# Kernel optimization log

Measured on AMD Instinct MI355X. Metric: run time of the kernel, lower is better.

The kernel has to match this reference:

```python
import jax, jax.numpy as jnp
import numpy as np

DIM = 192
HEADS = 6
WS = (2, 7, 7)
SHIFT = (1, 3, 3)
MLP_HID = int(DIM * 4.0)
N = WS[0] * WS[1] * WS[2]  # 98


def _relative_position_index():
    wt, wh, ww = WS
    coords = np.stack(np.meshgrid(np.arange(wt), np.arange(wh), np.arange(ww), indexing='ij'))
    cf = coords.reshape(3, -1)  # (3, N)
    rel = cf[:, :, None] - cf[:, None, :]  # (3, N, N)
    rel = rel.transpose(1, 2, 0).copy()
    rel[:, :, 0] += wt - 1
    rel[:, :, 1] += wh - 1
    rel[:, :, 2] += ww - 1
    rel[:, :, 0] *= (2 * wh - 1) * (2 * ww - 1)
    rel[:, :, 1] *= 2 * ww - 1
    return rel.sum(-1)  # (N, N) int

RPI = jnp.asarray(_relative_position_index())


def setup_inputs() -> dict:
    key = jax.random.key(0)
    ks = jax.random.split(key, 12)
    B, C, T, H, W = 2, DIM, 8, 56, 56
    n_bias = (2 * WS[0] - 1) * (2 * WS[1] - 1) * (2 * WS[2] - 1)
    s = lambda k, shp, sd=0.02: jax.random.normal(k, shp, jnp.float32) * sd
    return {
        'x': jax.random.normal(ks[0], (B, C, T, H, W), jnp.float32),
        'mask_matrix': jnp.zeros((256, N, N), jnp.float32),
        'norm1_g': jnp.ones((DIM,), jnp.float32),
        'norm1_b': jnp.zeros((DIM,), jnp.float32),
        'qkv_w': s(ks[1], (DIM, 3 * DIM)),
        'qkv_b': jnp.zeros((3 * DIM,), jnp.float32),
        'proj_w': s(ks[2], (DIM, DIM)),
        'proj_b': jnp.zeros((DIM,), jnp.float32),
        'rpb_table': s(ks[3], (n_bias, HEADS)),
        'norm2_g': jnp.ones((DIM,), jnp.float32),
        'norm2_b': jnp.zeros((DIM,), jnp.float32),
        'fc1_w': s(ks[4], (DIM, MLP_HID)),
        'fc1_b': jnp.zeros((MLP_HID,), jnp.float32),
        'fc2_w': s(ks[5], (MLP_HID, DIM)),
        'fc2_b': jnp.zeros((DIM,), jnp.float32),
    }


def _layernorm(x, g, b, eps=1e-5):
    mu = jnp.mean(x, -1, keepdims=True)
    var = jnp.var(x, -1, keepdims=True)
    return (x - mu) * jax.lax.rsqrt(var + eps) * g + b


def _window_partition(x):
    # x: (B, T, H, W, C) -> (B*nW, N, C)
    B, T, H, W, C = x.shape
    wt, wh, ww = WS
    x = x.reshape(B, T // wt, wt, H // wh, wh, W // ww, ww, C)
    x = x.transpose(0, 1, 3, 5, 2, 4, 6, 7)
    return x.reshape(-1, wt * wh * ww, C)


def _window_reverse(win, B, T, H, W):
    wt, wh, ww = WS
    C = win.shape[-1]
    x = win.reshape(B, T // wt, H // wh, W // ww, wt, wh, ww, C)
    x = x.transpose(0, 1, 4, 2, 5, 3, 6, 7)
    return x.reshape(B, T, H, W, C)


def reference(x, mask_matrix, norm1_g, norm1_b, qkv_w, qkv_b, proj_w, proj_b,
              rpb_table, norm2_g, norm2_b, fc1_w, fc1_b, fc2_w, fc2_b):
    B, C, T, H, W = x.shape
    hd = C // HEADS
    scale = hd ** -0.5

    shortcut = x.transpose(0, 2, 3, 4, 1)  # (B,T,H,W,C) channel-last residual
    xn = _layernorm(shortcut, norm1_g, norm1_b)
    # cyclic shift
    xs = jnp.roll(xn, shift=(-SHIFT[0], -SHIFT[1], -SHIFT[2]), axis=(1, 2, 3))
    xw = _window_partition(xs)  # (B_, N, C)
    B_ = xw.shape[0]

    qkv = (xw @ qkv_w + qkv_b).reshape(B_, N, 3, HEADS, hd)
    q, k, v = (qkv[:, :, 0].transpose(0, 2, 1, 3),
               qkv[:, :, 1].transpose(0, 2, 1, 3),
               qkv[:, :, 2].transpose(0, 2, 1, 3))  # (B_, h, N, d)
    attn = jnp.einsum('bhnd,bhmd->bhnm', q * scale, k)
    bias = rpb_table[RPI.reshape(-1)].reshape(N, N, HEADS).transpose(2, 0, 1)
    attn = attn + bias[None]
    nW = mask_matrix.shape[0]
    attn = attn.reshape(B_ // nW, nW, HEADS, N, N) + mask_matrix[None, :, None]
    attn = jax.nn.softmax(attn.reshape(B_, HEADS, N, N), axis=-1)
    out = jnp.einsum('bhnm,bhmd->bhnd', attn, v).transpose(0, 2, 1, 3).reshape(B_, N, C)
    out = out @ proj_w + proj_b

    xr = _window_reverse(out, B, T, H, W)
    xr = jnp.roll(xr, shift=SHIFT, axis=(1, 2, 3))
    x1 = shortcut + xr

    xn2 = _layernorm(x1, norm2_g, norm2_b)
    h1 = jax.nn.gelu(xn2 @ fc1_w + fc1_b, approximate=False)
    x2 = x1 + (h1 @ fc2_w + fc2_b)
    return x2.transpose(0, 4, 1, 2, 3)  # (B, C, T, H, W)
```

## Files before the change

kernel.cpp:

```cpp
#include <hip/hip_runtime.h>
#include <hip/hip_bf16.h>
#include <math.h>

#define DEV __device__ __forceinline__

typedef __bf16 bf16;
typedef __bf16 bf16x8 __attribute__((ext_vector_type(8)));
typedef float f32x4 __attribute__((ext_vector_type(4)));

DEV f32x4 zero4() { f32x4 z; z[0]=0.f; z[1]=0.f; z[2]=0.f; z[3]=0.f; return z; }

DEV void gload_lds16(const bf16* g, bf16* l) {
    __builtin_amdgcn_global_load_lds(
        (const __attribute__((address_space(1))) void*)g,
        (__attribute__((address_space(3))) void*)l, 16, 0, 0);
}

DEV float gelu_f(float v) {
    float e = __expf(-1.702f * v);
    return v * __builtin_amdgcn_rcpf(1.0f + e);
}

DEV f32x4 bmfma(bf16x8 a, bf16x8 b, f32x4 c) {
    return __builtin_amdgcn_mfma_f32_16x16x32_bf16(a, b, c, 0, 0, 0);
}


__global__ __launch_bounds__(256) void prep_all_k(
    const float* __restrict__ qw, const float* __restrict__ pw,
    const float* __restrict__ f1, const float* __restrict__ f2,
    const float* __restrict__ rpb, const float* __restrict__ maskm,
    bf16* __restrict__ qwt, bf16* __restrict__ pwt,
    bf16* __restrict__ f1t, bf16* __restrict__ f2t,
    float* __restrict__ biasF, float* __restrict__ maskF,
    int* __restrict__ wflag)
{
    int bid = blockIdx.x;
    if (bid < 3136) {
        int i = bid * 256 + threadIdx.x;
        if (i >= 256*7*7*64) return;
        int lane = i & 63; int g = i >> 6;
        int j = g % 7; g /= 7; int rt = g % 7; int wib = g / 7;
        int l15 = lane & 15, lg = lane >> 4;
        int nk = j*16 + l15;
        f32x4 o;
        #pragma unroll
        for (int r = 0; r < 4; r++) {
            int nq = rt*16 + lg*4 + r; if (nq > 97) nq = 97;
            o[r] = (nk < 98) ? maskm[((size_t)wib*98 + nq)*98 + nk] : 0.f;
        }
        *(f32x4*)&maskF[(size_t)i*4] = o;
    } else if (bid < 3712) {
        int i = (bid - 3136) * 256 + threadIdx.x;
        if (i < 576*192) { int n = i / 192, k = i % 192; qwt[i] = (bf16)qw[(size_t)k*576 + n]; }
        if (i < 192*192) { int n = i / 192, k = i % 192; pwt[i] = (bf16)pw[(size_t)k*192 + n]; }
        if (i < 768*192) { int n = i / 192, k = i % 192; f1t[i] = (bf16)f1[(size_t)k*768 + n]; }
        if (i < 192*768) { int n = i / 768, k = i % 768; f2t[i] = (bf16)f2[(size_t)k*192 + n]; }
    } else if (bid < 3786) {
        int i = (bid - 3712) * 256 + threadIdx.x;
        if (i >= 6*7*7*64) return;
        int lane = i & 63; int g = i >> 6;
        int j = g % 7; g /= 7; int rt = g % 7; int head = g / 7;
        int l15 = lane & 15, lg = lane >> 4;
        int nk = j*16 + l15;
        f32x4 o;
        #pragma unroll
        for (int r = 0; r < 4; r++) {
            int nq = rt*16 + lg*4 + r; if (nq > 97) nq = 97;
            if (nk < 98) {
                int t1 = nq/49, r1 = nq%49, h1 = r1/7, w1 = r1%7;
                int t2 = nk/49, r2 = nk%49, h2 = r2/7, w2 = r2%7;
                int idx = (t1 - t2 + 1)*169 + (h1 - h2 + 6)*13 + (w1 - w2 + 6);
                o[r] = rpb[idx*6 + head];
            } else {
                o[r] = -1e30f;
            }
        }
        *(f32x4*)&biasF[(size_t)i*4] = o;
    } else {
        __shared__ int f;
        int wib = bid - 3786;
        if (threadIdx.x == 0) f = 0;
        __syncthreads();
        int any = 0;
        const float* mm = maskm + (size_t)wib*9604;
        for (int i = threadIdx.x; i < 9604; i += 256)
            if (mm[i] != 0.f) any = 1;
        if (any) atomicOr(&f, 1);
        __syncthreads();
        if (threadIdx.x == 0) wflag[wib] = f;
    }
}

__global__ __launch_bounds__(256) void ln1_window_k(
    const float* __restrict__ x, const float* __restrict__ g,
    const float* __restrict__ bta, bf16* __restrict__ xw)
{
    __shared__ float tile[56*193];
    __shared__ float mu[56], rs[56];
    int blk = blockIdx.x;
    int bb = blk / 448; int r = blk % 448; int ts = r / 56; int hs = r % 56;
    int t = (ts + 1) & 7;
    int h = hs + 3; if (h >= 56) h -= 56;
    int tid = threadIdx.x;
    const float* xs = x + ((size_t)bb*1536 + t)*3136 + h*56;
    for (int e = tid; e < 192*56; e += 256) {
        int c = e / 56, w = e % 56;
        int wsp = w - 3; if (wsp < 0) wsp += 56;
        tile[wsp*193 + c] = xs[(size_t)c*25088 + w];
    }
    __syncthreads();
    if (tid < 224) {
        int row = tid >> 2, q = tid & 3;
        float s = 0.f, s2 = 0.f;
        for (int c = q*48; c < q*48 + 48; c++) {
            float v = tile[row*193 + c]; s += v; s2 += v*v;
        }
        s  += __shfl_xor(s, 1);  s  += __shfl_xor(s, 2);
        s2 += __shfl_xor(s2, 1); s2 += __shfl_xor(s2, 2);
        if (q == 0) {
            float m = s * (1.0f/192.0f);
            mu[row] = m;
            rs[row] = rsqrtf(s2 * (1.0f/192.0f) - m*m + 1e-5f);
        }
    }
    __syncthreads();
    int tb = ts >> 1, wt = ts & 1;
    int hb = hs / 7, wh = hs % 7;
    for (int e = tid; e < 56*192; e += 256) {
        int wpos = e / 192, c = e % 192;
        float v = (tile[wpos*193 + c] - mu[wpos]) * rs[wpos] * g[c] + bta[c];
        int wb = wpos / 7, ww = wpos % 7;
        int widx = bb*256 + tb*64 + hb*8 + wb;
        int n = wt*49 + wh*7 + ww;
        xw[((size_t)widx*98 + n)*192 + c] = (bf16)v;
    }
}

template<int KT, int NT, int BN, int EPI, int DB>
__global__ __launch_bounds__(256) void gemm_k(
    const bf16* __restrict__ A, const bf16* __restrict__ BT,
    const float* __restrict__ bias, const float* __restrict__ resid,
    void* __restrict__ outp)
{
    constexpr int BUFS = DB ? 2 : 1;
    __shared__ bf16 smem[BUFS*128*64 + BUFS*BN*64];
    bf16* laB = smem;
    bf16* lbB = smem + BUFS*128*64;
    constexpr int NTILES = NT / BN;
    constexpr int NK = KT / 64;
    constexpr int JT = BN / 32;
    constexpr int WN = BN / 2;
    constexpr int SPX = 392 / 8;
    int blk = blockIdx.x;
    int xcd = blk & 7, ix = blk >> 3;
    int m0 = (xcd * SPX + ix / NTILES) * 128;
    int n0 = (ix % NTILES) * BN;
    int tid = threadIdx.x;
    int lane = tid & 63;
    int wv = tid >> 6;
    int wr = wv >> 1, wc = wv & 1;
    int l15 = lane & 15, lg = lane >> 4;

    auto stage = [&](int kt, int buf) {
        int kb = kt * 64;
        #pragma unroll
        for (int t = 0; t < 4; t++) {
            int e = t*256 + wv*64 + lane;
            int row = e >> 3, ck = e & 7;
            gload_lds16(&A[(size_t)(m0 + row)*KT + kb + ((ck ^ (row & 7)) << 3)],
                        &laB[buf*128*64 + (t*256 + wv*64) * 8]);
        }
        #pragma unroll
        for (int t = 0; t < JT; t++) {
            int e = t*256 + wv*64 + lane;
            int row = e >> 3, ck = e & 7;
            gload_lds16(&BT[(size_t)(n0 + row)*KT + kb + ((ck ^ (row & 7)) << 3)],
                        &lbB[buf*BN*64 + (t*256 + wv*64) * 8]);
        }
    };

    f32x4 acc[4][JT];
    #pragma unroll
    for (int i = 0; i < 4; i++)
        #pragma unroll
        for (int j = 0; j < JT; j++) acc[i][j] = zero4();

    auto compute = [&](int cur) {
        const bf16* lab = laB + cur*128*64;
        const bf16* lbb = lbB + cur*BN*64;
        #pragma unroll
        for (int ks = 0; ks < 64; ks += 32) {
            int lc = (ks >> 3) + lg;
            bf16x8 af[4], bfr[JT];
            #pragma unroll
            for (int i = 0; i < 4; i++) {
                int ri = wr*64 + i*16 + l15;
                af[i] = *(const bf16x8*)&lab[ri*64 + ((lc ^ (ri & 7)) << 3)];
            }
            #pragma unroll
            for (int j = 0; j < JT; j++) {
                int rj = wc*WN + j*16 + l15;
                bfr[j] = *(const bf16x8*)&lbb[rj*64 + ((lc ^ (rj & 7)) << 3)];
            }
            #pragma unroll
            for (int i = 0; i < 4; i++)
                #pragma unroll
                for (int j = 0; j < JT; j++)
                    acc[i][j] = bmfma(af[i], bfr[j], acc[i][j]);
        }
    };

    if constexpr (DB) {
        stage(0, 0);
        __syncthreads();
        for (int kt = 0; kt < NK; kt++) {
            int cur = kt & 1;
            if (kt + 1 < NK) stage(kt + 1, cur ^ 1);
            compute(cur);
            __syncthreads();
        }
    } else {
        for (int kt = 0; kt < NK; kt++) {
            stage(kt, 0);
            __syncthreads();
            compute(0);
            __syncthreads();
        }
    }

    if constexpr (EPI == 4) {
        #pragma unroll
        for (int i = 0; i < 4; i++) {
            #pragma unroll
            for (int j = 0; j < JT; j++) {
                int row0 = m0 + wr*64 + i*16 + lg*4;
                int col = n0 + wc*WN + j*16 + l15;
                f32x4 o;
                #pragma unroll
                for (int r = 0; r < 4; r++)
                    o[r] = acc[i][j][r] + bias[col] + resid[(size_t)(row0 + r)*NT + col];
                int bb2 = row0 >= 25088;
                size_t off = (size_t)bb2*192*25088 + (size_t)col*25088 + (row0 - bb2*25088);
                *(f32x4*)&((float*)outp)[off] = o;
            }
        }
    } else if constexpr (EPI == 5) {
        #pragma unroll
        for (int i = 0; i < 4; i++) {
            #pragma unroll
            for (int j = 0; j < JT; j++) {
                int col = n0 + wc*WN + j*16 + l15;
                int sel = col / 192, hd = (col % 192) >> 5, d = col & 31;
                float bv = bias[col];
                #pragma unroll
                for (int r = 0; r < 4; r++) {
                    int row = m0 + wr*64 + i*16 + lg*4 + r;
                    int b_ = row / 98, n = row - b_*98;
                    size_t dst = (((size_t)b_*6 + hd)*3 + sel)*3136 + n*32 + d;
                    ((bf16*)outp)[dst] = (bf16)(acc[i][j][r] + bv);
                }
            }
        }
    } else if constexpr (EPI == 1 || EPI == 0) {
        #pragma unroll
        for (int i = 0; i < 4; i++) {
            #pragma unroll
            for (int j = 0; j < JT; j++) {
                #pragma unroll
                for (int r = 0; r < 4; r++) {
                    int row = m0 + wr*64 + i*16 + lg*4 + r;
                    int col = n0 + wc*WN + j*16 + l15;
                    float v = acc[i][j][r] + bias[col];
                    if constexpr (EPI == 1)
                        ((float*)outp)[(size_t)row*NT + col] = v;
                    else
                        ((bf16*)outp)[(size_t)row*NT + col] = (bf16)v;
                }
            }
        }
    } else {
        bf16* fs = smem;
        #pragma unroll
        for (int i = 0; i < 4; i++) {
            #pragma unroll
            for (int j = 0; j < JT; j++) {
                int colw = wc*WN + j*16 + l15;
                float bv = bias[n0 + colw];
                #pragma unroll
                for (int r = 0; r < 4; r++) {
                    int lr = wr*64 + i*16 + lg*4 + r;
                    fs[lr*72 + colw] = (bf16)gelu_f(acc[i][j][r] + bv);
                }
            }
        }
        __syncthreads();
        {
            int lr = tid >> 1, c0 = (tid & 1) * 32;
            size_t gbase = (size_t)(m0 + lr)*NT + n0 + c0;
            #pragma unroll
            for (int k = 0; k < 4; k++) {
                bf16x8 o = *(const bf16x8*)&fs[lr*72 + c0 + k*8];
                *(bf16x8*)&((bf16*)outp)[gbase + k*8] = o;
            }
        }
    }
}

__global__ __launch_bounds__(128) void attn_k(
    const bf16* __restrict__ qkv, const float* __restrict__ biasF,
    const float* __restrict__ maskF, const int* __restrict__ wflag,
    bf16* __restrict__ aout)
{
    __shared__ bf16 VT[32*128];
    __shared__ bf16 Pl[2*16*136];
    int blk = blockIdx.x;
    int t8 = (blk & 7) * 384 + (blk >> 3);
    int b_ = t8 / 6, head = t8 % 6;
    int tid = threadIdx.x, lane = tid & 63, wv = tid >> 6;
    int l15 = lane & 15, lg = (lane >> 4) & 3;
    int wib = b_ & 255;
    const bf16* base = qkv + (size_t)(b_*6 + head)*3*3136;
    const int hasmask = wflag[wib];

    {
        unsigned int* vz = (unsigned int*)VT;
        for (int e = tid; e < 2048; e += 128) vz[e] = 0u;
        unsigned int* pz = (unsigned int*)Pl;
        for (int e = tid; e < 256; e += 128) {
            int w2 = e >> 7, rem = e & 127;
            int row = rem >> 3, cp = rem & 7;
            pz[(w2*16 + row)*68 + 56 + cp] = 0u;
        }
    }
    __syncthreads();
    {
        int dq = tid >> 5;
        int kl = tid & 31;
        const bf16* vbase = base + 2*3136 + dq*8;
        #pragma unroll
        for (int kr = 0; kr < 4; kr++) {
            int k = kr*32 + kl;
            if (k < 98) {
                bf16x8 v8 = *(const bf16x8*)&vbase[k*32];
                #pragma unroll
                for (int j = 0; j < 8; j++)
                    VT[(dq*8 + j)*128 + (k ^ (j << 3))] = v8[j];
            }
        }
    }
    __syncthreads();

    bf16x8 kfr[7];
    #pragma unroll
    for (int j = 0; j < 7; j++) {
        int krow = j*16 + l15; if (krow > 97) krow = 97;
        kfr[j] = *(const bf16x8*)&base[3136 + krow*32 + lg*8];
    }

    const float scale = 0.17677669529663687f;
    bf16* Pw = Pl + wv*16*136;
    const int rt0 = wv ? 4 : 0, rt1 = wv ? 7 : 4;

    auto loadQ = [&](int rt) {
        int qrow = rt*16 + l15; if (qrow > 97) qrow = 97;
        return *(const bf16x8*)&base[qrow*32 + lg*8];
    };
    bf16x8 qf = loadQ(rt0);

    #pragma unroll 1
    for (int rt = rt0; rt < rt1; rt++) {
        bf16x8 qnext = qf;
        if (rt + 1 < rt1) qnext = loadQ(rt + 1);
        f32x4 sacc[7];
        #pragma unroll
        for (int j = 0; j < 7; j++) sacc[j] = zero4();
        #pragma unroll
        for (int j = 0; j < 7; j++)
            sacc[j] = bmfma(qf, kfr[j], sacc[j]);
        {
            const float* bfp = biasF + ((size_t)(head*7 + rt)*7)*256 + lane*4;
            #pragma unroll
            for (int j = 0; j < 7; j++) {
                f32x4 bv = *(const f32x4*)&bfp[j*256];
                sacc[j] = sacc[j]*scale + bv;
            }
            if (hasmask) {
                const float* mfp = maskF + ((size_t)(wib*7 + rt)*7)*256 + lane*4;
                #pragma unroll
                for (int j = 0; j < 7; j++) {
                    f32x4 mv = *(const f32x4*)&mfp[j*256];
                    sacc[j] = sacc[j] + mv;
                }
            }
            f32x4 m4 = sacc[0];
            #pragma unroll
            for (int j = 1; j < 7; j++) {
                #pragma unroll
                for (int r = 0; r < 4; r++) m4[r] = fmaxf(m4[r], sacc[j][r]);
            }
            #pragma unroll
            for (int d = 1; d < 16; d <<= 1) {
                #pragma unroll
                for (int r = 0; r < 4; r++) m4[r] = fmaxf(m4[r], __shfl_xor(m4[r], d));
            }
            f32x4 s4 = zero4();
            #pragma unroll
            for (int j = 0; j < 7; j++) {
                #pragma unroll
                for (int r = 0; r < 4; r++) sacc[j][r] = __expf(sacc[j][r] - m4[r]);
                s4 += sacc[j];
            }
            #pragma unroll
            for (int d = 1; d < 16; d <<= 1) {
                #pragma unroll
                for (int r = 0; r < 4; r++) s4[r] += __shfl_xor(s4[r], d);
            }
            f32x4 inv4;
            #pragma unroll
            for (int r = 0; r < 4; r++) inv4[r] = 1.0f / s4[r];
            #pragma unroll
            for (int j = 0; j < 7; j++)
                #pragma unroll
                for (int r = 0; r < 4; r++)
                    Pw[(lg*4 + r)*136 + j*16 + l15] = (bf16)(sacc[j][r]*inv4[r]);
        }
        #pragma unroll
        for (int dt = 0; dt < 2; dt++) {
            int dl = dt*16 + l15;
            int xr = (dl & 7) << 3;
            f32x4 oacc = zero4();
            #pragma unroll
            for (int kc = 0; kc < 4; kc++) {
                bf16x8 pf = *(const bf16x8*)&Pw[l15*136 + kc*32 + lg*8];
                bf16x8 vf = *(const bf16x8*)&VT[dl*128 + ((kc*32 + lg*8) ^ xr)];
                oacc = bmfma(pf, vf, oacc);
            }
            #pragma unroll
            for (int r = 0; r < 4; r++) {
                int row = rt*16 + lg*4 + r;
                if (row < 98)
                    aout[((size_t)b_*98 + row)*192 + head*32 + dt*16 + l15] = (bf16)oacc[r];
            }
        }
        qf = qnext;
    }
}

__global__ __launch_bounds__(256) void rev_res_ln2_k(
    const float* __restrict__ x, const bf16* __restrict__ pw,
    const float* __restrict__ g2, const float* __restrict__ b2,
    float* __restrict__ x1, bf16* __restrict__ xn2)
{
    __shared__ float tile[56*193];
    __shared__ float mu[56], rs[56];
    int blk = blockIdx.x;
    int bb = blk / 448; int r = blk % 448; int t = r / 56; int h = r % 56;
    int ts = (t + 7) & 7;
    int hs = h - 3; if (hs < 0) hs += 56;
    int tid = threadIdx.x;
    const float* xs = x + ((size_t)bb*1536 + t)*3136 + h*56;
    for (int e = tid; e < 192*56; e += 256) {
        int c = e / 56, w = e % 56;
        tile[w*193 + c] = xs[(size_t)c*25088 + w];
    }
    __syncthreads();
    int tb = ts >> 1, wt = ts & 1, hb = hs / 7, wh = hs % 7;
    for (int e = tid; e < 56*192; e += 256) {
        int w = e / 192, c = e % 192;
        int wsp = w - 3; if (wsp < 0) wsp += 56;
        int wb = wsp / 7, ww = wsp % 7;
        size_t tok = (size_t)(bb*256 + tb*64 + hb*8 + wb)*98 + wt*49 + wh*7 + ww;
        tile[w*193 + c] += (float)pw[tok*192 + c];
    }
    __syncthreads();
    if (tid < 224) {
        int row = tid >> 2, q = tid & 3;
        float s = 0.f, s2 = 0.f;
        for (int c = q*48; c < q*48 + 48; c++) {
            float v = tile[row*193 + c]; s += v; s2 += v*v;
        }
        s  += __shfl_xor(s, 1);  s  += __shfl_xor(s, 2);
        s2 += __shfl_xor(s2, 1); s2 += __shfl_xor(s2, 2);
        if (q == 0) {
            float m = s * (1.0f/192.0f);
            mu[row] = m;
            rs[row] = rsqrtf(s2 * (1.0f/192.0f) - m*m + 1e-5f);
        }
    }
    __syncthreads();
    size_t tok0 = ((size_t)(bb*8 + t)*56 + h)*56;
    for (int e = tid; e < 56*192; e += 256) {
        int w = e / 192, c = e % 192;
        float v = tile[w*193 + c];
        x1[(tok0 + w)*192 + c] = v;
        xn2[(tok0 + w)*192 + c] = (bf16)((v - mu[w]) * rs[w] * g2[c] + b2[c]);
    }
}

extern "C" void kernel_launch(void* const* d_in, const int* in_sizes, int n_in,
                              void* d_out, int out_size, void* d_ws, size_t ws_size,
                              hipStream_t stream)
{
    const float* x     = (const float*)d_in[0];
    const float* maskm = (const float*)d_in[1];
    const float* n1g   = (const float*)d_in[2];
    const float* n1b   = (const float*)d_in[3];
    const float* qkvw  = (const float*)d_in[4];
    const float* qkvb  = (const float*)d_in[5];
    const float* projw = (const float*)d_in[6];
    const float* projb = (const float*)d_in[7];
    const float* rpb   = (const float*)d_in[8];
    const float* n2g   = (const float*)d_in[9];
    const float* n2b   = (const float*)d_in[10];
    const float* f1w   = (const float*)d_in[11];
    const float* f1b   = (const float*)d_in[12];
    const float* f2w   = (const float*)d_in[13];
    const float* f2b   = (const float*)d_in[14];

    char* ws = (char*)d_ws;
    int*   wflag   = (int*)(ws + 0);
    bf16*  qkv_wt  = (bf16*)(ws + 1024);
    bf16*  proj_wt = (bf16*)(ws + 222208);
    bf16*  fc1_wt  = (bf16*)(ws + 295936);
    bf16*  fc2_wt  = (bf16*)(ws + 590848);
    float* biasF   = (float*)(ws + 885760);
    bf16* xw   = (bf16*)(ws + 1180672);
    bf16* aout = xw;
    char* Bp = ws + 1180672 + 19267584;
    bf16*  qkv  = (bf16*)Bp;
    bf16*  pwin = (bf16*)Bp;
    char* Cp = Bp + 57802752;
    float* x1  = (float*)Cp;
    bf16*  xn2 = (bf16*)(Cp + 38535168);
    bf16*  h1  = (bf16*)(Cp + 38535168 + 19267584);
    float* maskF = (float*)(Cp + 38535168 + 19267584);

    prep_all_k<<<4042, 256, 0, stream>>>(qkvw, projw, f1w, f2w, rpb, maskm,
                                         qkv_wt, proj_wt, fc1_wt, fc2_wt,
                                         biasF, maskF, wflag);
    ln1_window_k<<<896, 256, 0, stream>>>(x, n1g, n1b, xw);
    gemm_k<192, 576, 192, 5, 0><<<392*3, 256, 0, stream>>>(xw, qkv_wt, qkvb, nullptr, qkv);
    attn_k<<<3072, 128, 0, stream>>>(qkv, biasF, maskF, wflag, aout);
    gemm_k<192, 192, 64, 0, 0><<<392*3, 256, 0, stream>>>(aout, proj_wt, projb, nullptr, pwin);
    rev_res_ln2_k<<<896, 256, 0, stream>>>(x, pwin, n2g, n2b, x1, xn2);
    gemm_k<192, 768, 64, 2, 0><<<392*12, 256, 0, stream>>>(xn2, fc1_wt, f1b, nullptr, h1);
    gemm_k<768, 192, 64, 4, 1><<<392*3, 256, 0, stream>>>(h1, fc2_wt, f2b, x1, (float*)d_out);
}
```

Baseline: 233.3 us.

## Store residual in bf16, skip mask expansion for zero windows, LDS-staged proj epilogue

The mask-flag computation moves into its own kernel ahead of prep, so prep can skip writing the expanded mask tile for windows whose mask is all zero. The residual x1 is now stored in bf16 instead of fp32, which halves its write and its read in the final GEMM epilogue, at some precision cost on the residual path. The projection GEMM switches to the LDS-staged epilogue path (EPI 3, gelu off) for coalesced bf16 stores. The cost is one extra kernel launch.

```diff
diff --git a/kernel.cpp b/kernel.cpp
--- a/kernel.cpp
+++ b/kernel.cpp
@@ -25,6 +25,22 @@
     return __builtin_amdgcn_mfma_f32_16x16x32_bf16(a, b, c, 0, 0, 0);
 }
 
+
+__global__ __launch_bounds__(256) void prep_flag_k(
+    const float* __restrict__ maskm, int* __restrict__ wflag)
+{
+    __shared__ int f;
+    int wib = blockIdx.x;
+    if (threadIdx.x == 0) f = 0;
+    __syncthreads();
+    int any = 0;
+    const float* mm = maskm + (size_t)wib*9604;
+    for (int i = threadIdx.x; i < 9604; i += 256)
+        if (mm[i] != 0.f) any = 1;
+    if (any) atomicOr(&f, 1);
+    __syncthreads();
+    if (threadIdx.x == 0) wflag[wib] = f;
+}
 
 __global__ __launch_bounds__(256) void prep_all_k(
     const float* __restrict__ qw, const float* __restrict__ pw,
@@ -33,7 +49,7 @@
     bf16* __restrict__ qwt, bf16* __restrict__ pwt,
     bf16* __restrict__ f1t, bf16* __restrict__ f2t,
     float* __restrict__ biasF, float* __restrict__ maskF,
-    int* __restrict__ wflag)
+    const int* __restrict__ wflag)
 {
     int bid = blockIdx.x;
     if (bid < 3136) {
@@ -41,6 +57,7 @@
         if (i >= 256*7*7*64) return;
         int lane = i & 63; int g = i >> 6;
         int j = g % 7; g /= 7; int rt = g % 7; int wib = g / 7;
+        if (wflag[wib] == 0) return;
         int l15 = lane & 15, lg = lane >> 4;
         int nk = j*16 + l15;
         f32x4 o;
@@ -56,7 +73,7 @@
         if (i < 192*192) { int n = i / 192, k = i % 192; pwt[i] = (bf16)pw[(size_t)k*192 + n]; }
         if (i < 768*192) { int n = i / 192, k = i % 192; f1t[i] = (bf16)f1[(size_t)k*768 + n]; }
         if (i < 192*768) { int n = i / 768, k = i % 768; f2t[i] = (bf16)f2[(size_t)k*192 + n]; }
-    } else if (bid < 3786) {
+    } else {
         int i = (bid - 3712) * 256 + threadIdx.x;
         if (i >= 6*7*7*64) return;
         int lane = i & 63; int g = i >> 6;
@@ -77,18 +94,6 @@
             }
         }
         *(f32x4*)&biasF[(size_t)i*4] = o;
-    } else {
-        __shared__ int f;
-        int wib = bid - 3786;
-        if (threadIdx.x == 0) f = 0;
-        __syncthreads();
-        int any = 0;
-        const float* mm = maskm + (size_t)wib*9604;
-        for (int i = threadIdx.x; i < 9604; i += 256)
-            if (mm[i] != 0.f) any = 1;
-        if (any) atomicOr(&f, 1);
-        __syncthreads();
-        if (threadIdx.x == 0) wflag[wib] = f;
     }
 }
 
@@ -140,7 +145,7 @@
 template<int KT, int NT, int BN, int EPI, int DB>
 __global__ __launch_bounds__(256) void gemm_k(
     const bf16* __restrict__ A, const bf16* __restrict__ BT,
-    const float* __restrict__ bias, const float* __restrict__ resid,
+    const float* __restrict__ bias, const void* __restrict__ resid,
     void* __restrict__ outp)
 {
     constexpr int BUFS = DB ? 2 : 1;
@@ -230,6 +235,7 @@
     }
 
     if constexpr (EPI == 4) {
+        const bf16* rs = (const bf16*)resid;
         #pragma unroll
         for (int i = 0; i < 4; i++) {
             #pragma unroll
@@ -239,7 +245,7 @@
                 f32x4 o;
                 #pragma unroll
                 for (int r = 0; r < 4; r++)
-                    o[r] = acc[i][j][r] + bias[col] + resid[(size_t)(row0 + r)*NT + col];
+                    o[r] = acc[i][j][r] + bias[col] + (float)rs[(size_t)(row0 + r)*NT + col];
                 int bb2 = row0 >= 25088;
                 size_t off = (size_t)bb2*192*25088 + (size_t)col*25088 + (row0 - bb2*25088);
                 *(f32x4*)&((float*)outp)[off] = o;
@@ -262,7 +268,7 @@
                 }
             }
         }
-    } else if constexpr (EPI == 1 || EPI == 0) {
+    } else if constexpr (EPI == 1) {
         #pragma unroll
         for (int i = 0; i < 4; i++) {
             #pragma unroll
@@ -271,11 +277,7 @@
                 for (int r = 0; r < 4; r++) {
                     int row = m0 + wr*64 + i*16 + lg*4 + r;
                     int col = n0 + wc*WN + j*16 + l15;
-                    float v = acc[i][j][r] + bias[col];
-                    if constexpr (EPI == 1)
-                        ((float*)outp)[(size_t)row*NT + col] = v;
-                    else
-                        ((bf16*)outp)[(size_t)row*NT + col] = (bf16)v;
+                    ((float*)outp)[(size_t)row*NT + col] = acc[i][j][r] + bias[col];
                 }
             }
         }
@@ -290,7 +292,9 @@
                 #pragma unroll
                 for (int r = 0; r < 4; r++) {
                     int lr = wr*64 + i*16 + lg*4 + r;
-                    fs[lr*72 + colw] = (bf16)gelu_f(acc[i][j][r] + bv);
+                    float v = acc[i][j][r] + bv;
+                    if constexpr (EPI == 2) v = gelu_f(v);
+                    fs[lr*72 + colw] = (bf16)v;
                 }
             }
         }
@@ -450,7 +454,7 @@
 __global__ __launch_bounds__(256) void rev_res_ln2_k(
     const float* __restrict__ x, const bf16* __restrict__ pw,
     const float* __restrict__ g2, const float* __restrict__ b2,
-    float* __restrict__ x1, bf16* __restrict__ xn2)
+    bf16* __restrict__ x1, bf16* __restrict__ xn2)
 {
     __shared__ float tile[56*193];
     __shared__ float mu[56], rs[56];
@@ -493,7 +497,7 @@
     for (int e = tid; e < 56*192; e += 256) {
         int w = e / 192, c = e % 192;
         float v = tile[w*193 + c];
-        x1[(tok0 + w)*192 + c] = v;
+        x1[(tok0 + w)*192 + c] = (bf16)v;
         xn2[(tok0 + w)*192 + c] = (bf16)((v - mu[w]) * rs[w] * g2[c] + b2[c]);
     }
 }
@@ -531,18 +535,19 @@
     bf16*  qkv  = (bf16*)Bp;
     bf16*  pwin = (bf16*)Bp;
     char* Cp = Bp + 57802752;
-    float* x1  = (float*)Cp;
-    bf16*  xn2 = (bf16*)(Cp + 38535168);
-    bf16*  h1  = (bf16*)(Cp + 38535168 + 19267584);
-    float* maskF = (float*)(Cp + 38535168 + 19267584);
-
-    prep_all_k<<<4042, 256, 0, stream>>>(qkvw, projw, f1w, f2w, rpb, maskm,
+    bf16*  x1  = (bf16*)Cp;
+    bf16*  xn2 = (bf16*)(Cp + 19267584);
+    bf16*  h1  = (bf16*)(Cp + 19267584 + 19267584);
+    float* maskF = (float*)(Cp + 19267584 + 19267584);
+
+    prep_flag_k<<<256, 256, 0, stream>>>(maskm, wflag);
+    prep_all_k<<<3786, 256, 0, stream>>>(qkvw, projw, f1w, f2w, rpb, maskm,
                                          qkv_wt, proj_wt, fc1_wt, fc2_wt,
                                          biasF, maskF, wflag);
     ln1_window_k<<<896, 256, 0, stream>>>(x, n1g, n1b, xw);
     gemm_k<192, 576, 192, 5, 0><<<392*3, 256, 0, stream>>>(xw, qkv_wt, qkvb, nullptr, qkv);
     attn_k<<<3072, 128, 0, stream>>>(qkv, biasF, maskF, wflag, aout);
-    gemm_k<192, 192, 64, 0, 0><<<392*3, 256, 0, stream>>>(aout, proj_wt, projb, nullptr, pwin);
+    gemm_k<192, 192, 64, 3, 0><<<392*3, 256, 0, stream>>>(aout, proj_wt, projb, nullptr, pwin);
     rev_res_ln2_k<<<896, 256, 0, stream>>>(x, pwin, n2g, n2b, x1, xn2);
     gemm_k<192, 768, 64, 2, 0><<<392*12, 256, 0, stream>>>(xn2, fc1_wt, f1b, nullptr, h1);
     gemm_k<768, 192, 64, 4, 1><<<392*3, 256, 0, stream>>>(h1, fc2_wt, f2b, x1, (float*)d_out);
```

New measurement: 229.9 us. Within noise of the previous version (-1.5%).
